# Performance work log

Hardware: AMD Instinct MI355X
Metric: run time of the kernel (lower is better)

Reference implementation:

```python
import jax, jax.numpy as jnp
import numpy as np

N = 100000
NEG_SLOPE = 0.2
EPS = 1e-16


def gat_conv(x, edge_index, W, att_src, att_dst, bias, concat):
    # x: [N, Fin]; W: [Fin, H*C]; att_*: [H, C]; edge_index: [2, E] (with self loops)
    H, C = att_src.shape
    src, dst = edge_index[0], edge_index[1]
    h = (x @ W).reshape(-1, H, C)                       # [N, H, C]
    a_src = (h * att_src).sum(-1)                       # [N, H]
    a_dst = (h * att_dst).sum(-1)                       # [N, H]
    e = a_src[src] + a_dst[dst]                         # [E, H]
    e = jnp.where(e >= 0, e, NEG_SLOPE * e)             # LeakyReLU(0.2)
    # segment softmax over destination-node neighborhoods
    m = jax.ops.segment_max(e, dst, num_segments=N)     # [N, H]
    ex = jnp.exp(e - m[dst])
    denom = jax.ops.segment_sum(ex, dst, num_segments=N)
    alpha = ex / (denom[dst] + EPS)                     # [E, H]
    msg = h[src] * alpha[:, :, None]                    # [E, H, C]
    out = jax.ops.segment_sum(msg, dst, num_segments=N)  # [N, H, C]
    out = out.reshape(N, H * C) if concat else out.mean(axis=1)
    return out + bias


def setup_inputs() -> dict:
    key = jax.random.key(0)
    ks = jax.random.split(key, 10)
    Fin, Ch, Co, Hh = 256, 32, 64, 4
    E = 1600000
    x = jax.random.normal(ks[0], (N, Fin), dtype=jnp.float32)
    edge_index = jax.random.randint(ks[1], (2, E), 0, N, dtype=jnp.int64)
    s1 = 1.0 / np.sqrt(Fin)
    s2 = 1.0 / np.sqrt(Hh * Ch)
    W1 = jax.random.normal(ks[2], (Fin, Hh * Ch), dtype=jnp.float32) * s1
    att_src1 = jax.random.normal(ks[3], (Hh, Ch), dtype=jnp.float32) * (1.0 / np.sqrt(Ch))
    att_dst1 = jax.random.normal(ks[4], (Hh, Ch), dtype=jnp.float32) * (1.0 / np.sqrt(Ch))
    b1 = jnp.zeros((Hh * Ch,), dtype=jnp.float32)
    W2 = jax.random.normal(ks[5], (Hh * Ch, Co), dtype=jnp.float32) * s2
    att_src2 = jax.random.normal(ks[6], (1, Co), dtype=jnp.float32) * (1.0 / np.sqrt(Co))
    att_dst2 = jax.random.normal(ks[7], (1, Co), dtype=jnp.float32) * (1.0 / np.sqrt(Co))
    b2 = jnp.zeros((Co,), dtype=jnp.float32)
    return {"x": x, "edge_index": edge_index,
            "W1": W1, "att_src1": att_src1, "att_dst1": att_dst1, "b1": b1,
            "W2": W2, "att_src2": att_src2, "att_dst2": att_dst2, "b2": b2}


def reference(x, edge_index, W1, att_src1, att_dst1, b1, W2, att_src2, att_dst2, b2):
    # add self-loops (PyG GATConv default add_self_loops=True)
    loops = jnp.arange(N, dtype=edge_index.dtype)
    ei = jnp.concatenate([edge_index, jnp.stack([loops, loops])], axis=1)
    h = gat_conv(x, ei, W1, att_src1, att_dst1, b1, concat=True)
    h = jax.nn.elu(h)
    out = gat_conv(h, ei, W2, att_src2, att_dst2, b2, concat=False)
    return out
```

## Files before the change

### kernel.cpp

```cpp
#include <hip/hip_runtime.h>
#include <math.h>

typedef unsigned short ushort_t;
typedef unsigned int uint_t;
typedef __attribute__((ext_vector_type(8))) short short8;
typedef __attribute__((ext_vector_type(4))) float fx4;
typedef __attribute__((ext_vector_type(4))) uint_t uintx4;
typedef __attribute__((ext_vector_type(2))) uint_t uintx2;

__device__ __forceinline__ float bf16_to_f32(ushort_t u) {
    union { uint_t i; float f; } c;
    c.i = ((uint_t)u) << 16;
    return c.f;
}
__device__ __forceinline__ ushort_t f32_to_bf16(float f) {
    union { float f; uint_t i; } c;
    c.f = f;
    const uint_t x = c.i;
    return (ushort_t)((x + 0x7fffu + ((x >> 16) & 1u)) >> 16);
}
__device__ __forceinline__ void unpack_fma(uint_t w, float p, float& a0,
                                           float& a1) {
    union { uint_t i; float f; } lo, hi;
    lo.i = w << 16;
    hi.i = w & 0xffff0000u;
    a0 += p * lo.f;
    a1 += p * hi.f;
}

__global__ void convT_kernel(const float* __restrict__ W,
                             ushort_t* __restrict__ WT, int k, int m) {
    const int idx = blockIdx.x * 256 + threadIdx.x;
    if (idx >= k * m) return;
    const int mm = idx / k;
    const int kk = idx % k;
    WT[idx] = f32_to_bf16(W[(size_t)kk * m + mm]);
}

template <int TILES, bool A_F32, int K, int KS>
__global__ __launch_bounds__(256) void gemm_lds_kernel(
    const void* __restrict__ Avoid, const ushort_t* __restrict__ BT,
    ushort_t* __restrict__ C, int n) {
    constexpr int M = TILES * 16;
    constexpr int CHS = KS / 8;
    constexpr int NCS = KS / 32;
    constexpr int NC = K / 32;
    __shared__ ushort_t lds[M * KS];
    const int tid = threadIdx.x;
    const int wave = tid >> 6;
    const int lane = tid & 63;
    const int l15 = lane & 15;
    const int quad = lane >> 4;
    const int rowbase = blockIdx.x * 128 + wave * 32;
    const int r0 = min(rowbase + l15, n - 1);
    const int r1 = min(rowbase + 16 + l15, n - 1);
    const size_t off0 = (size_t)r0 * K + quad * 8;
    const size_t off1 = (size_t)r1 * K + quad * 8;

    fx4 acc[2][TILES];
#pragma unroll
    for (int rp = 0; rp < 2; ++rp)
#pragma unroll
        for (int t = 0; t < TILES; ++t) acc[rp][t] = (fx4){0.f, 0.f, 0.f, 0.f};

    fx4 c0a, c0b, c1a, c1b, n0a, n0b, n1a, n1b;
    short8 cb0, cb1, nb0, nb1;

    if constexpr (A_F32) {
        const float* A = (const float*)Avoid;
        c0a = *(const fx4*)(A + off0);
        c0b = *(const fx4*)(A + off0 + 4);
        c1a = *(const fx4*)(A + off1);
        c1b = *(const fx4*)(A + off1 + 4);
    } else {
        const ushort_t* A = (const ushort_t*)Avoid;
        cb0 = *(const short8*)(A + off0);
        cb1 = *(const short8*)(A + off1);
    }

#pragma unroll
    for (int ks = 0; ks < K; ks += KS) {
        if (ks) __syncthreads();
#pragma unroll
        for (int i = 0; i < (M * CHS + 255) / 256; ++i) {
            const int idx = tid + i * 256;
            if (idx < M * CHS) {
                const int row = idx / CHS;
                const int c = idx - row * CHS;
                *(short8*)&lds[(size_t)(row * CHS + (c ^ (row & 7))) * 8] =
                    *(const short8*)(BT + (size_t)row * K + ks + c * 8);
            }
        }
        __syncthreads();

#pragma unroll
        for (int kc = 0; kc < NCS; ++kc) {
            const int kg = ks / 32 + kc;
            if (kg + 1 < NC) {
                const int kd = (kg + 1) * 32;
                if constexpr (A_F32) {
                    const float* A = (const float*)Avoid;
                    n0a = *(const fx4*)(A + off0 + kd);
                    n0b = *(const fx4*)(A + off0 + kd + 4);
                    n1a = *(const fx4*)(A + off1 + kd);
                    n1b = *(const fx4*)(A + off1 + kd + 4);
                } else {
                    const ushort_t* A = (const ushort_t*)Avoid;
                    nb0 = *(const short8*)(A + off0 + kd);
                    nb1 = *(const short8*)(A + off1 + kd);
                }
            }
            short8 bf[TILES];
#pragma unroll
            for (int t = 0; t < TILES; ++t) {
                const int brow = t * 16 + l15;
                const int c = kc * 4 + quad;
                bf[t] = *(const short8*)&lds[(size_t)(brow * CHS +
                                                      (c ^ (brow & 7))) * 8];
            }
            short8 af0, af1;
            if constexpr (A_F32) {
                union { short8 v; ushort_t u[8]; } u0, u1;
#pragma unroll
                for (int j = 0; j < 4; ++j) {
                    u0.u[j] = f32_to_bf16(c0a[j]);
                    u0.u[4 + j] = f32_to_bf16(c0b[j]);
                    u1.u[j] = f32_to_bf16(c1a[j]);
                    u1.u[4 + j] = f32_to_bf16(c1b[j]);
                }
                af0 = u0.v;
                af1 = u1.v;
            } else {
                af0 = cb0;
                af1 = cb1;
            }
#pragma unroll
            for (int t = 0; t < TILES; ++t) {
                acc[0][t] = __builtin_amdgcn_mfma_f32_16x16x32_bf16(
                    af0, bf[t], acc[0][t], 0, 0, 0);
                acc[1][t] = __builtin_amdgcn_mfma_f32_16x16x32_bf16(
                    af1, bf[t], acc[1][t], 0, 0, 0);
            }
            if (kg + 1 < NC) {
                if constexpr (A_F32) {
                    c0a = n0a; c0b = n0b; c1a = n1a; c1b = n1b;
                } else {
                    cb0 = nb0; cb1 = nb1;
                }
            }
        }
    }

#pragma unroll
    for (int rp = 0; rp < 2; ++rp) {
        const int crow0 = rowbase + rp * 16 + quad * 4;
#pragma unroll
        for (int t = 0; t < TILES; ++t) {
#pragma unroll
            for (int r = 0; r < 4; ++r) {
                const int rr = crow0 + r;
                if (rr < n)
                    C[(size_t)rr * M + t * 16 + l15] =
                        f32_to_bf16(acc[rp][t][r]);
            }
        }
    }
}

template <int H, int C>
__global__ void att_kernel(const ushort_t* __restrict__ h,
                           const float* __restrict__ att_s,
                           const float* __restrict__ att_d,
                           float* __restrict__ as_, float* __restrict__ ad_,
                           int n) {
    const int idx = blockIdx.x * blockDim.x + threadIdx.x;
    if (idx >= n * H) return;
    const int node = idx / H;
    const int hh = idx % H;
    const ushort_t* hp = h + (size_t)node * H * C + hh * C;
    float s0 = 0.f, s1 = 0.f;
#pragma unroll
    for (int c = 0; c < C; ++c) {
        const float v = bf16_to_f32(hp[c]);
        s0 += v * att_s[hh * C + c];
        s1 += v * att_d[hh * C + c];
    }
    as_[idx] = s0;
    ad_[idx] = s1;
}

__global__ __launch_bounds__(1024) void hist_kernel(const int* __restrict__ dst,
                                                    int* __restrict__ histG,
                                                    int e, int chunk, int NB,
                                                    int G) {
    __shared__ int hl[512];
    for (int b = threadIdx.x; b < NB; b += 1024) hl[b] = 0;
    __syncthreads();
    const int g = blockIdx.x;
    const int lo = g * chunk;
    const int hi = min(lo + chunk, e);
    for (int i = lo + threadIdx.x; i < hi; i += 1024)
        atomicAdd(&hl[dst[i] >> 8], 1);
    __syncthreads();
    for (int b = threadIdx.x; b < NB; b += 1024) histG[b * G + g] = hl[b];
}

__global__ __launch_bounds__(1024) void scan1_kernel(const int* __restrict__ in,
                                                     int* __restrict__ out,
                                                     int* __restrict__ sums,
                                                     int n) {
    __shared__ int s[1024];
    const int t = threadIdx.x;
    const int i = blockIdx.x * 1024 + t;
    const int v = (i < n) ? in[i] : 0;
    s[t] = v;
    __syncthreads();
    for (int d = 1; d < 1024; d <<= 1) {
        const int x = (t >= d) ? s[t - d] : 0;
        __syncthreads();
        s[t] += x;
        __syncthreads();
    }
    if (i < n) out[i] = s[t] - v;
    if (t == 1023) sums[blockIdx.x] = s[1023];
}

__global__ __launch_bounds__(128) void scan2_kernel(int* sums, int nb) {
    __shared__ int s[128];
    const int t = threadIdx.x;
    const int v = (t < nb) ? sums[t] : 0;
    s[t] = v;
    __syncthreads();
    for (int d = 1; d < 128; d <<= 1) {
        const int x = (t >= d) ? s[t - d] : 0;
        __syncthreads();
        s[t] += x;
        __syncthreads();
    }
    if (t < nb) sums[t] = s[t] - v;
}

__global__ __launch_bounds__(1024) void scan3_kernel(int* __restrict__ out,
                                                     const int* __restrict__ sums,
                                                     int n) {
    const int i = blockIdx.x * 1024 + threadIdx.x;
    if (i < n) out[i] += sums[blockIdx.x];
}

__global__ __launch_bounds__(1024) void bin_kernel(const int* __restrict__ src,
                                                   const int* __restrict__ dst,
                                                   const int* __restrict__ base,
                                                   int2* __restrict__ binned,
                                                   int e, int chunk, int NB,
                                                   int G) {
    __shared__ int cur[512];
    const int g = blockIdx.x;
    for (int b = threadIdx.x; b < NB; b += 1024) cur[b] = base[b * G + g];
    __syncthreads();
    const int lo = g * chunk;
    const int hi = min(lo + chunk, e);
    for (int i = lo + threadIdx.x; i < hi; i += 1024) {
        const int d = dst[i];
        const int p = atomicAdd(&cur[d >> 8], 1);
        binned[p] = make_int2(src[i], d);
    }
}

#define BUILD_CAP 6144
__global__ __launch_bounds__(256) void build_kernel(
    const int2* __restrict__ binned, const int* __restrict__ base,
    int* __restrict__ csr, int* __restrict__ deg, int* __restrict__ offs,
    int e, int n, int NB, int G) {
    __shared__ int2 ep[BUILD_CAP];
    __shared__ int degL[256];
    __shared__ int offL[256];
    __shared__ int curL[256];
    const int b = blockIdx.x;
    const int tid = threadIdx.x;
    const int start = base[b * G];
    const int end = (b == NB - 1) ? e : base[(b + 1) * G];
    const int cnt = end - start;
    const bool stage = (cnt <= BUILD_CAP);
    degL[tid] = 0;
    if (stage)
        for (int i = tid; i < cnt; i += 256) ep[i] = binned[start + i];
    __syncthreads();
    if (stage) {
        for (int i = tid; i < cnt; i += 256) atomicAdd(&degL[ep[i].y & 255], 1);
    } else {
        for (int i = tid; i < cnt; i += 256)
            atomicAdd(&degL[binned[start + i].y & 255], 1);
    }
    __syncthreads();
    const int v = degL[tid];
    offL[tid] = v;
    __syncthreads();
    for (int d = 1; d < 256; d <<= 1) {
        const int x = (tid >= d) ? offL[tid - d] : 0;
        __syncthreads();
        offL[tid] += x;
        __syncthreads();
    }
    const int excl = offL[tid] - v;
    curL[tid] = excl;
    const int node = (b << 8) + tid;
    if (node < n) {
        deg[node] = v;
        offs[node] = start + excl;
    }
    __syncthreads();
    if (stage) {
        for (int i = tid; i < cnt; i += 256) {
            const int p = atomicAdd(&curL[ep[i].y & 255], 1);
            csr[start + p] = ep[i].x;
        }
    } else {
        for (int i = tid; i < cnt; i += 256) {
            const int2 pr = binned[start + i];
            const int p = atomicAdd(&curL[pr.y & 255], 1);
            csr[start + p] = pr.x;
        }
    }
}

template <int H, int C, bool DO_ELU, bool OUT_BF16>
__global__ __launch_bounds__(64) void agg_kernel(
    const ushort_t* __restrict__ h, const float* __restrict__ a_src,
    const float* __restrict__ a_dst, const int* __restrict__ csr,
    const int* __restrict__ offs, const int* __restrict__ deg,
    const float* __restrict__ bias, void* __restrict__ outv, int n) {
    constexpr int HC = H * C;
    constexpr int R = HC / 16;
    constexpr int RW = R / 2;
    constexpr int U = 4;
    const int lane = threadIdx.x;
    const int s = lane & 15;
    const int g = lane >> 4;
    const int dst = blockIdx.x * 4 + g;
    const int dstc = min(dst, n - 1);
    const int start = offs[dstc];
    const int dg = deg[dstc];
    const int ch0 = s * R;
    const int myh = (H > 1) ? (ch0 / C) : 0;
    const float advm = a_dst[dstc * H + myh];

    int dmax = dg;
    dmax = max(dmax, __shfl_xor(dmax, 16));
    dmax = max(dmax, __shfl_xor(dmax, 32));
    dmax = __builtin_amdgcn_readfirstlane(dmax);

    float acc[R];
#pragma unroll
    for (int r = 0; r < R; ++r) acc[r] = 0.f;
    float L = 0.f;

    {
        float e = a_src[dstc * H + myh] + advm;
        e = fmaxf(e, 0.2f * e);
        const float p = __expf(e);
        L += p;
        const ushort_t* hp = h + (size_t)((uint_t)dstc * HC) + ch0;
        if constexpr (RW == 4) {
            const uintx4 v = *(const uintx4*)hp;
#pragma unroll
            for (int w = 0; w < 4; ++w)
                unpack_fma(v[w], p, acc[2 * w], acc[2 * w + 1]);
        } else {
            const uintx2 v = *(const uintx2*)hp;
#pragma unroll
            for (int w = 0; w < 2; ++w)
                unpack_fma(v[w], p, acc[2 * w], acc[2 * w + 1]);
        }
    }

    const int dm1c = (dg > 0) ? dg - 1 : 0;

    for (int j0 = 0; j0 < dmax; j0 += U) {
        int sv[U];
#pragma unroll
        for (int u = 0; u < U; ++u)
            sv[u] = csr[start + min(j0 + u, dm1c)];
        float es[U];
#pragma unroll
        for (int u = 0; u < U; ++u) es[u] = a_src[sv[u] * H + myh];
        uint_t hv[U][RW];
#pragma unroll
        for (int u = 0; u < U; ++u) {
            const ushort_t* hp = h + (size_t)((uint_t)sv[u] * HC) + ch0;
            if constexpr (RW == 4) {
                const uintx4 v = *(const uintx4*)hp;
#pragma unroll
                for (int w = 0; w < 4; ++w) hv[u][w] = v[w];
            } else {
                const uintx2 v = *(const uintx2*)hp;
#pragma unroll
                for (int w = 0; w < 2; ++w) hv[u][w] = v[w];
            }
        }
        float p[U];
#pragma unroll
        for (int u = 0; u < U; ++u) {
            float e = es[u] + advm;
            e = fmaxf(e, 0.2f * e);
            const float pe = __expf(e);
            p[u] = (j0 + u < dg) ? pe : 0.f;
        }
#pragma unroll
        for (int u = 0; u < U; ++u) {
            L += p[u];
#pragma unroll
            for (int w = 0; w < RW; ++w)
                unpack_fma(hv[u][w], p[u], acc[2 * w], acc[2 * w + 1]);
        }
    }

    if (dst >= n) return;
    const float linv = 1.f / (L + 1e-16f);
    float r[R];
#pragma unroll
    for (int d = 0; d < R; ++d) {
        r[d] = acc[d] * linv + bias[ch0 + d];
        if (DO_ELU) r[d] = (r[d] > 0.f) ? r[d] : (__expf(r[d]) - 1.f);
    }
    if constexpr (OUT_BF16) {
        uintx4 o;
#pragma unroll
        for (int w = 0; w < 4; ++w)
            o[w] = (uint_t)f32_to_bf16(r[2 * w]) |
                   ((uint_t)f32_to_bf16(r[2 * w + 1]) << 16);
        *(uintx4*)((ushort_t*)outv + (size_t)dst * HC + ch0) = o;
    } else {
        fx4 o;
#pragma unroll
        for (int d = 0; d < 4; ++d) o[d] = r[d];
        *(fx4*)((float*)outv + (size_t)dst * HC + ch0) = o;
    }
}

extern "C" void kernel_launch(void* const* d_in, const int* in_sizes, int n_in,
                              void* d_out, int out_size, void* d_ws,
                              size_t ws_size, hipStream_t stream) {
    const float* x = (const float*)d_in[0];
    const int* ei = (const int*)d_in[1];
    const float* W1 = (const float*)d_in[2];
    const float* att_s1 = (const float*)d_in[3];
    const float* att_d1 = (const float*)d_in[4];
    const float* b1 = (const float*)d_in[5];
    const float* W2 = (const float*)d_in[6];
    const float* att_s2 = (const float*)d_in[7];
    const float* att_d2 = (const float*)d_in[8];
    const float* b2 = (const float*)d_in[9];

    const int N = in_sizes[0] / 256;
    const int E = in_sizes[1] / 2;
    const int* srcp = ei;
    const int* dstp = ei + E;

    const int NB = (N + 255) >> 8;
    const int G = 128;
    const int NBG = NB * G;
    const int chunk = (E + G - 1) / G;
    const int nbs = (NBG + 1023) / 1024;

    float* as1 = (float*)d_ws;
    float* ad1 = as1 + (size_t)N * 4;
    float* as2 = ad1 + (size_t)N * 4;
    float* ad2 = as2 + N;
    int* histG = (int*)(ad2 + N);
    int* base = histG + NBG;
    int* sums = base + NBG;
    int* deg = sums + 128;
    int* offs = deg + N;
    int* csr = offs + N;
    int2* binned = (int2*)(csr + E);
    ushort_t* h1 = (ushort_t*)binned;
    ushort_t* h2 = h1 + (size_t)N * 128;
    ushort_t* h1p = h2 + (size_t)N * 64;
    ushort_t* W1T = h1p + (size_t)N * 128;
    ushort_t* W2T = W1T + 128 * 256;

    convT_kernel<<<(256 * 128 + 255) / 256, 256, 0, stream>>>(W1, W1T, 256, 128);
    convT_kernel<<<(128 * 64 + 255) / 256, 256, 0, stream>>>(W2, W2T, 128, 64);

    hist_kernel<<<G, 1024, 0, stream>>>(dstp, histG, E, chunk, NB, G);
    scan1_kernel<<<nbs, 1024, 0, stream>>>(histG, base, sums, NBG);
    scan2_kernel<<<1, 128, 0, stream>>>(sums, nbs);
    scan3_kernel<<<nbs, 1024, 0, stream>>>(base, sums, NBG);
    bin_kernel<<<G, 1024, 0, stream>>>(srcp, dstp, base, binned, E, chunk, NB,
                                       G);
    build_kernel<<<NB, 256, 0, stream>>>(binned, base, csr, deg, offs, E, N,
                                         NB, G);

    const int gblk = (N + 127) / 128;
    const int ablk = (N + 3) / 4;

    gemm_lds_kernel<8, true, 256, 128><<<gblk, 256, 0, stream>>>(x, W1T, h1,
                                                                 N);
    att_kernel<4, 32><<<(N * 4 + 255) / 256, 256, 0, stream>>>(h1, att_s1,
                                                               att_d1, as1,
                                                               ad1, N);
    agg_kernel<4, 32, true, true><<<ablk, 64, 0, stream>>>(h1, as1, ad1, csr,
                                                           offs, deg, b1, h1p,
                                                           N);

    gemm_lds_kernel<4, false, 128, 128><<<gblk, 256, 0, stream>>>(h1p, W2T,
                                                                  h2, N);
    att_kernel<1, 64><<<(N + 255) / 256, 256, 0, stream>>>(h2, att_s2, att_d2,
                                                           as2, ad2, N);
    agg_kernel<1, 64, false, false><<<ablk, 64, 0, stream>>>(h2, as2, ad2,
                                                             csr, offs, deg,
                                                             b2, d_out, N);
}
```

Measured before the change: 390.5 us.

## Use 32x32 MFMA GEMM tiles, pack binned edges into 32 bits, merge weight conversions

Replaces the 16x16x32 MFMA GEMM with a 32x32x16 variant that handles 256 rows per block, aiming for more reuse per B-fragment load and fewer blocks. The binned edge records go from int2 to a single uint holding a 17-bit source index and the low 8 bits of the destination, which halves binning traffic and LDS footprint in the CSR build. The two weight-transpose launches become one kernel. Packing assumes node ids fit in 17 bits (N=100000), and the larger accumulator arrays raise register pressure.

New measurement: 385.4 us. Within noise of the previous version (-1.3%).

```diff
diff --git a/kernel.cpp b/kernel.cpp
--- a/kernel.cpp
+++ b/kernel.cpp
@@ -5,6 +5,7 @@
 typedef unsigned int uint_t;
 typedef __attribute__((ext_vector_type(8))) short short8;
 typedef __attribute__((ext_vector_type(4))) float fx4;
+typedef __attribute__((ext_vector_type(16))) float f32x16;
 typedef __attribute__((ext_vector_type(4))) uint_t uintx4;
 typedef __attribute__((ext_vector_type(2))) uint_t uintx2;
 
@@ -28,40 +29,50 @@
     a1 += p * hi.f;
 }
 
-__global__ void convT_kernel(const float* __restrict__ W,
-                             ushort_t* __restrict__ WT, int k, int m) {
+__global__ void convT2_kernel(const float* __restrict__ W1,
+                              ushort_t* __restrict__ W1T,
+                              const float* __restrict__ W2,
+                              ushort_t* __restrict__ W2T) {
     const int idx = blockIdx.x * 256 + threadIdx.x;
-    if (idx >= k * m) return;
-    const int mm = idx / k;
-    const int kk = idx % k;
-    WT[idx] = f32_to_bf16(W[(size_t)kk * m + mm]);
-}
-
-template <int TILES, bool A_F32, int K, int KS>
-__global__ __launch_bounds__(256) void gemm_lds_kernel(
+    if (idx < 256 * 128) {
+        const int mm = idx / 256;
+        const int kk = idx - mm * 256;
+        W1T[idx] = f32_to_bf16(W1[(size_t)kk * 128 + mm]);
+    } else if (idx < 256 * 128 + 128 * 64) {
+        const int j = idx - 256 * 128;
+        const int mm = j / 128;
+        const int kk = j - mm * 128;
+        W2T[j] = f32_to_bf16(W2[(size_t)kk * 64 + mm]);
+    }
+}
+
+template <int TILES32, bool A_F32, int K, int KS>
+__global__ __launch_bounds__(256) void gemm32_kernel(
     const void* __restrict__ Avoid, const ushort_t* __restrict__ BT,
     ushort_t* __restrict__ C, int n) {
-    constexpr int M = TILES * 16;
+    constexpr int M = TILES32 * 32;
     constexpr int CHS = KS / 8;
-    constexpr int NCS = KS / 32;
-    constexpr int NC = K / 32;
+    constexpr int NSTEP = KS / 16;
+    constexpr int NTOT = K / 16;
     __shared__ ushort_t lds[M * KS];
     const int tid = threadIdx.x;
     const int wave = tid >> 6;
     const int lane = tid & 63;
-    const int l15 = lane & 15;
-    const int quad = lane >> 4;
-    const int rowbase = blockIdx.x * 128 + wave * 32;
-    const int r0 = min(rowbase + l15, n - 1);
-    const int r1 = min(rowbase + 16 + l15, n - 1);
-    const size_t off0 = (size_t)r0 * K + quad * 8;
-    const size_t off1 = (size_t)r1 * K + quad * 8;
-
-    fx4 acc[2][TILES];
+    const int l31 = lane & 31;
+    const int half = lane >> 5;
+    const int rowbase = blockIdx.x * 256 + wave * 64;
+    const int r0 = min(rowbase + l31, n - 1);
+    const int r1 = min(rowbase + 32 + l31, n - 1);
+    const size_t off0 = (size_t)r0 * K + half * 8;
+    const size_t off1 = (size_t)r1 * K + half * 8;
+
+    f32x16 acc[2][TILES32];
 #pragma unroll
     for (int rp = 0; rp < 2; ++rp)
 #pragma unroll
-        for (int t = 0; t < TILES; ++t) acc[rp][t] = (fx4){0.f, 0.f, 0.f, 0.f};
+        for (int t = 0; t < TILES32; ++t)
+#pragma unroll
+            for (int i = 0; i < 16; ++i) acc[rp][t][i] = 0.f;
 
     fx4 c0a, c0b, c1a, c1b, n0a, n0b, n1a, n1b;
     short8 cb0, cb1, nb0, nb1;
@@ -87,17 +98,18 @@
             if (idx < M * CHS) {
                 const int row = idx / CHS;
                 const int c = idx - row * CHS;
-                *(short8*)&lds[(size_t)(row * CHS + (c ^ (row & 7))) * 8] =
+                *(short8*)&lds[(size_t)(row * CHS +
+                                        (c ^ (row & (CHS - 1)))) * 8] =
                     *(const short8*)(BT + (size_t)row * K + ks + c * 8);
             }
         }
         __syncthreads();
 
 #pragma unroll
-        for (int kc = 0; kc < NCS; ++kc) {
-            const int kg = ks / 32 + kc;
-            if (kg + 1 < NC) {
-                const int kd = (kg + 1) * 32;
+        for (int kstep = 0; kstep < NSTEP; ++kstep) {
+            const int kg = ks / 16 + kstep;
+            if (kg + 1 < NTOT) {
+                const int kd = (kg + 1) * 16;
                 if constexpr (A_F32) {
                     const float* A = (const float*)Avoid;
                     n0a = *(const fx4*)(A + off0 + kd);
@@ -110,13 +122,14 @@
                     nb1 = *(const short8*)(A + off1 + kd);
                 }
             }
-            short8 bf[TILES];
-#pragma unroll
-            for (int t = 0; t < TILES; ++t) {
-                const int brow = t * 16 + l15;
-                const int c = kc * 4 + quad;
+            short8 bf[TILES32];
+#pragma unroll
+            for (int t = 0; t < TILES32; ++t) {
+                const int brow = t * 32 + l31;
+                const int c = kstep * 2 + half;
                 bf[t] = *(const short8*)&lds[(size_t)(brow * CHS +
-                                                      (c ^ (brow & 7))) * 8];
+                                                      (c ^ (brow &
+                                                            (CHS - 1)))) * 8];
             }
             short8 af0, af1;
             if constexpr (A_F32) {
@@ -135,13 +148,13 @@
                 af1 = cb1;
             }
 #pragma unroll
-            for (int t = 0; t < TILES; ++t) {
-                acc[0][t] = __builtin_amdgcn_mfma_f32_16x16x32_bf16(
+            for (int t = 0; t < TILES32; ++t) {
+                acc[0][t] = __builtin_amdgcn_mfma_f32_32x32x16_bf16(
                     af0, bf[t], acc[0][t], 0, 0, 0);
-                acc[1][t] = __builtin_amdgcn_mfma_f32_16x16x32_bf16(
+                acc[1][t] = __builtin_amdgcn_mfma_f32_32x32x16_bf16(
                     af1, bf[t], acc[1][t], 0, 0, 0);
             }
-            if (kg + 1 < NC) {
+            if (kg + 1 < NTOT) {
                 if constexpr (A_F32) {
                     c0a = n0a; c0b = n0b; c1a = n1a; c1b = n1b;
                 } else {
@@ -153,15 +166,15 @@
 
 #pragma unroll
     for (int rp = 0; rp < 2; ++rp) {
-        const int crow0 = rowbase + rp * 16 + quad * 4;
-#pragma unroll
-        for (int t = 0; t < TILES; ++t) {
-#pragma unroll
-            for (int r = 0; r < 4; ++r) {
-                const int rr = crow0 + r;
+        const int base_r = rowbase + rp * 32 + 4 * half;
+#pragma unroll
+        for (int t = 0; t < TILES32; ++t) {
+            const int col = t * 32 + l31;
+#pragma unroll
+            for (int reg = 0; reg < 16; ++reg) {
+                const int rr = base_r + (reg & 3) + 8 * (reg >> 2);
                 if (rr < n)
-                    C[(size_t)rr * M + t * 16 + l15] =
-                        f32_to_bf16(acc[rp][t][r]);
+                    C[(size_t)rr * M + col] = f32_to_bf16(acc[rp][t][reg]);
             }
         }
     }
@@ -250,7 +263,7 @@
 __global__ __launch_bounds__(1024) void bin_kernel(const int* __restrict__ src,
                                                    const int* __restrict__ dst,
                                                    const int* __restrict__ base,
-                                                   int2* __restrict__ binned,
+                                                   uint_t* __restrict__ binned,
                                                    int e, int chunk, int NB,
                                                    int G) {
     __shared__ int cur[512];
@@ -262,16 +275,16 @@
     for (int i = lo + threadIdx.x; i < hi; i += 1024) {
         const int d = dst[i];
         const int p = atomicAdd(&cur[d >> 8], 1);
-        binned[p] = make_int2(src[i], d);
+        binned[p] = (uint_t)src[i] | ((uint_t)(d & 255) << 17);
     }
 }
 
 #define BUILD_CAP 6144
 __global__ __launch_bounds__(256) void build_kernel(
-    const int2* __restrict__ binned, const int* __restrict__ base,
+    const uint_t* __restrict__ binned, const int* __restrict__ base,
     int* __restrict__ csr, int* __restrict__ deg, int* __restrict__ offs,
     int e, int n, int NB, int G) {
-    __shared__ int2 ep[BUILD_CAP];
+    __shared__ uint_t ep[BUILD_CAP];
     __shared__ int degL[256];
     __shared__ int offL[256];
     __shared__ int curL[256];
@@ -286,10 +299,11 @@
         for (int i = tid; i < cnt; i += 256) ep[i] = binned[start + i];
     __syncthreads();
     if (stage) {
-        for (int i = tid; i < cnt; i += 256) atomicAdd(&degL[ep[i].y & 255], 1);
+        for (int i = tid; i < cnt; i += 256)
+            atomicAdd(&degL[ep[i] >> 17], 1);
     } else {
         for (int i = tid; i < cnt; i += 256)
-            atomicAdd(&degL[binned[start + i].y & 255], 1);
+            atomicAdd(&degL[binned[start + i] >> 17], 1);
     }
     __syncthreads();
     const int v = degL[tid];
@@ -311,14 +325,15 @@
     __syncthreads();
     if (stage) {
         for (int i = tid; i < cnt; i += 256) {
-            const int p = atomicAdd(&curL[ep[i].y & 255], 1);
-            csr[start + p] = ep[i].x;
+            const uint_t pr = ep[i];
+            const int p = atomicAdd(&curL[pr >> 17], 1);
+            csr[start + p] = (int)(pr & 0x1FFFFu);
         }
     } else {
         for (int i = tid; i < cnt; i += 256) {
-            const int2 pr = binned[start + i];
-            const int p = atomicAdd(&curL[pr.y & 255], 1);
-            csr[start + p] = pr.x;
+            const uint_t pr = binned[start + i];
+            const int p = atomicAdd(&curL[pr >> 17], 1);
+            csr[start + p] = (int)(pr & 0x1FFFFu);
         }
     }
 }
@@ -472,15 +487,15 @@
     int* deg = sums + 128;
     int* offs = deg + N;
     int* csr = offs + N;
-    int2* binned = (int2*)(csr + E);
+    uint_t* binned = (uint_t*)(csr + E);
     ushort_t* h1 = (ushort_t*)binned;
     ushort_t* h2 = h1 + (size_t)N * 128;
     ushort_t* h1p = h2 + (size_t)N * 64;
     ushort_t* W1T = h1p + (size_t)N * 128;
     ushort_t* W2T = W1T + 128 * 256;
 
-    convT_kernel<<<(256 * 128 + 255) / 256, 256, 0, stream>>>(W1, W1T, 256, 128);
-    convT_kernel<<<(128 * 64 + 255) / 256, 256, 0, stream>>>(W2, W2T, 128, 64);
+    convT2_kernel<<<(256 * 128 + 128 * 64 + 255) / 256, 256, 0, stream>>>(
+        W1, W1T, W2, W2T);
 
     hist_kernel<<<G, 1024, 0, stream>>>(dstp, histG, E, chunk, NB, G);
     scan1_kernel<<<nbs, 1024, 0, stream>>>(histG, base, sums, NBG);
@@ -491,11 +506,10 @@
     build_kernel<<<NB, 256, 0, stream>>>(binned, base, csr, deg, offs, E, N,
                                          NB, G);
 
-    const int gblk = (N + 127) / 128;
+    const int gblk = (N + 255) / 256;
     const int ablk = (N + 3) / 4;
 
-    gemm_lds_kernel<8, true, 256, 128><<<gblk, 256, 0, stream>>>(x, W1T, h1,
-                                                                 N);
+    gemm32_kernel<4, true, 256, 128><<<gblk, 256, 0, stream>>>(x, W1T, h1, N);
     att_kernel<4, 32><<<(N * 4 + 255) / 256, 256, 0, stream>>>(h1, att_s1,
                                                                att_d1, as1,
                                                                ad1, N);
@@ -503,8 +517,8 @@
                                                            offs, deg, b1, h1p,
                                                            N);
 
-    gemm_lds_kernel<4, false, 128, 128><<<gblk, 256, 0, stream>>>(h1p, W2T,
-                                                                  h2, N);
+    gemm32_kernel<2, false, 128, 128><<<gblk, 256, 0, stream>>>(h1p, W2T, h2,
+                                                                N);
     att_kernel<1, 64><<<(N + 255) / 256, 256, 0, stream>>>(h2, att_s2, att_d2,
                                                            as2, ad2, N);
     agg_kernel<1, 64, false, false><<<ablk, 64, 0, stream>>>(h2, as2, ad2,
```
